# Kernel tuning notes

Hardware: AMD Instinct MI355X
Metric: run time of the kernel (lower is better)

The kernel has to match this reference:

```python
import jax, jax.numpy as jnp
import numpy as np

N_NODES = 100000
N_EDGES = 1600000
IN_FEATS, HIDDEN, N_CLASSES = 128, 64, 16


def gcn_layer(x, src, dst, W, b, n_nodes):
    # DGL GraphConv, norm='both': h = D_in^{-1/2} A (D_out^{-1/2} x) W + b
    # (W applied before aggregation since in_feats > out_feats, as DGL does)
    ones = jnp.ones((src.shape[0],), dtype=x.dtype)
    deg_out = jax.ops.segment_sum(ones, src, num_segments=n_nodes)
    deg_in = jax.ops.segment_sum(ones, dst, num_segments=n_nodes)
    norm_src = jax.lax.rsqrt(jnp.clip(deg_out, 1.0))  # [N]
    norm_dst = jax.lax.rsqrt(jnp.clip(deg_in, 1.0))   # [N]
    h = (x * norm_src[:, None]) @ W                    # [N, out]
    msgs = h[src]                                      # [E, out] gather
    agg = jax.ops.segment_sum(msgs, dst, num_segments=n_nodes)  # [N, out]
    return agg * norm_dst[:, None] + b


def setup_inputs() -> dict:
    key = jax.random.key(0)
    k1, k2, k3, k4, k5, k6, k7 = jax.random.split(key, 7)
    x = jax.random.normal(k1, (N_NODES, IN_FEATS), dtype=jnp.float32)
    src = jax.random.randint(k2, (N_EDGES,), 0, N_NODES, dtype=jnp.int32)
    dst = jax.random.randint(k3, (N_EDGES,), 0, N_NODES, dtype=jnp.int32)
    s1 = 1.0 / np.sqrt(IN_FEATS)
    s2 = 1.0 / np.sqrt(HIDDEN)
    W1 = jax.random.uniform(k4, (IN_FEATS, HIDDEN), jnp.float32, -s1, s1)
    b1 = jnp.zeros((HIDDEN,), dtype=jnp.float32)
    W2 = jax.random.uniform(k5, (HIDDEN, N_CLASSES), jnp.float32, -s2, s2)
    b2 = jnp.zeros((N_CLASSES,), dtype=jnp.float32)
    return {"x": x, "src": src, "dst": dst, "W1": W1, "b1": b1, "W2": W2, "b2": b2}


def reference(x, src, dst, W1, b1, W2, b2):
    h = gcn_layer(x, src, dst, W1, b1, N_NODES)
    h = jax.nn.relu(h)
    h = gcn_layer(h, src, dst, W2, b2, N_NODES)
    return jax.nn.softmax(h, axis=-1)  # [N, num_classes]
```

## Files before the change

kernel.cpp:

```cpp
#include <hip/hip_runtime.h>
#include <hip/hip_fp16.h>
#include <math.h>


constexpr int N_NODES = 100000;
constexpr int N_EDGES = 1600000;
constexpr int IN_F    = 128;
constexpr int HID     = 64;
constexpr int NC      = 16;

constexpr int NB_D   = 391;
constexpr int STR    = 4608;
constexpr int NBLK_P = 256;
constexpr int EPB    = N_EDGES / NBLK_P;
constexpr int CAPB   = 64;
constexpr int CSTR   = 16;

typedef _Float16 f16x8 __attribute__((ext_vector_type(8)));
typedef _Float16 f16x4 __attribute__((ext_vector_type(4)));
typedef float    f32x4 __attribute__((ext_vector_type(4)));

__global__ __launch_bounds__(512) void k_init(int* __restrict__ cursD,
                                              int* __restrict__ cursS) {
    int t = threadIdx.x;
    if (t < NB_D) {
        cursD[t * CSTR] = t * STR;
        cursS[t * CSTR] = t * STR;
    }
}

__global__ __launch_bounds__(1024) void k_part(const int* __restrict__ src,
                                               const int* __restrict__ dst,
                                               int* __restrict__ cursD,
                                               int* __restrict__ cursS,
                                               unsigned int* __restrict__ ebufD,
                                               unsigned char* __restrict__ ebufS) {
    __shared__ unsigned int  bufD[NB_D * CAPB];
    __shared__ unsigned char bufS[NB_D * CAPB];
    __shared__ int cD[NB_D], cS[NB_D], baseD[NB_D], baseS[NB_D];
    const int t = threadIdx.x, b = blockIdx.x;
    for (int i = t; i < NB_D; i += 1024) { cD[i] = 0; cS[i] = 0; }
    __syncthreads();
    const int beg = b * EPB, end = beg + EPB;
    for (int i = beg + t; i < end; i += 1024) {
        int d = dst[i], s = src[i];
        int bD = d >> 8;
        int c  = atomicAdd(&cD[bD], 1);
        if (c < CAPB) bufD[(bD << 6) + c] = ((unsigned)(d & 255) << 17) | (unsigned)s;
        int bS = s >> 8;
        int c2 = atomicAdd(&cS[bS], 1);
        if (c2 < CAPB) bufS[(bS << 6) + c2] = (unsigned char)(s & 255);
    }
    __syncthreads();
    for (int i = t; i < NB_D; i += 1024) {
        int c = min(cD[i], CAPB);
        cD[i] = c;
        baseD[i] = atomicAdd(&cursD[i * CSTR], c);
        int c2 = min(cS[i], CAPB);
        cS[i] = c2;
        baseS[i] = atomicAdd(&cursS[i * CSTR], c2);
    }
    __syncthreads();
    for (int slot = t; slot < NB_D * CAPB; slot += 1024) {
        int bk = slot >> 6, idx = slot & 63;
        if (idx < cD[bk]) ebufD[baseD[bk] + idx] = bufD[slot];
    }
    for (int slot = t; slot < NB_D * CAPB; slot += 1024) {
        int bk = slot >> 6, idx = slot & 63;
        if (idx < cS[bk]) ebufS[baseS[bk] + idx] = bufS[slot];
    }
}

__global__ __launch_bounds__(256) void k_bmerge(const int* __restrict__ cursD,
                                                const int* __restrict__ cursS,
                                                const unsigned int* __restrict__ ebufD,
                                                const unsigned char* __restrict__ ebufS,
                                                int* __restrict__ row_start,
                                                int* __restrict__ row_end,
                                                float* __restrict__ norm_dst,
                                                float* __restrict__ norm_src,
                                                int* __restrict__ csr_src) {
    __shared__ int cnt[256];
    __shared__ int curs[256];
    __shared__ int wsum[4];
    const int t = threadIdx.x;
    int b = blockIdx.x;
    if (b < NB_D) {
        const int beg = b * STR, end = cursD[b * CSTR];
        cnt[t] = 0;
        __syncthreads();
        for (int i = beg + t; i < end; i += 256)
            atomicAdd(&cnt[ebufD[i] >> 17], 1);
        __syncthreads();
        int x = cnt[t];
        int v = x;
        int lane = t & 63, wid = t >> 6;
        #pragma unroll
        for (int d = 1; d < 64; d <<= 1) { int u = __shfl_up(v, d, 64); if (lane >= d) v += u; }
        if (lane == 63) wsum[wid] = v;
        __syncthreads();
        int woff = 0;
        for (int w = 0; w < wid; ++w) woff += wsum[w];
        int rs = woff + v - x;
        int node = b * 256 + t;
        if (node < N_NODES) {
            row_start[node] = beg + rs;
            row_end[node]   = beg + rs + x;
            norm_dst[node]  = 1.0f / sqrtf(fmaxf((float)x, 1.0f));
        }
        curs[t] = beg + rs;
        __syncthreads();
        for (int i = beg + t; i < end; i += 256) {
            unsigned int e = ebufD[i];
            int pos = atomicAdd(&curs[e >> 17], 1);
            csr_src[pos] = (int)(e & 0x1FFFFu);
        }
    } else {
        b -= NB_D;
        const int beg = b * STR, end = cursS[b * CSTR];
        cnt[t] = 0;
        __syncthreads();
        for (int i = beg + t; i < end; i += 256)
            atomicAdd(&cnt[ebufS[i]], 1);
        __syncthreads();
        int node = b * 256 + t;
        if (node < N_NODES)
            norm_src[node] = 1.0f / sqrtf(fmaxf((float)cnt[t], 1.0f));
    }
}

constexpr int PADK = 136;
__global__ __launch_bounds__(256) void k_gemm1(
        const float* __restrict__ x, const float* __restrict__ W1,
        const float* __restrict__ norm_src, __half* __restrict__ h1h) {
    __shared__ _Float16 xh[64 * PADK];
    __shared__ _Float16 wt[64 * PADK];
    const int t = threadIdx.x;
    const int row0 = blockIdx.x * 64;
    for (int i = t; i < 64 * 32; i += 256) {
        int c4 = i & 31, rr = i >> 5;
        int gr = row0 + rr;
        float4 v = (gr < N_NODES) ? *(const float4*)&x[(size_t)gr * IN_F + c4 * 4]
                                  : float4{0.f, 0.f, 0.f, 0.f};
        f16x4 hv;
        hv[0] = (_Float16)v.x; hv[1] = (_Float16)v.y;
        hv[2] = (_Float16)v.z; hv[3] = (_Float16)v.w;
        *(f16x4*)&xh[rr * PADK + c4 * 4] = hv;
    }
    for (int i = t; i < 64 * 32; i += 256) {
        int n = i & 63, kq = i >> 6;
        int k0 = kq * 4;
        f16x4 hv;
        #pragma unroll
        for (int j = 0; j < 4; ++j)
            hv[j] = (_Float16)W1[(size_t)(k0 + j) * HID + n];
        *(f16x4*)&wt[n * PADK + k0] = hv;
    }
    __syncthreads();
    const int w = t >> 6;
    const int l = t & 63;
    const int m = l & 15, q = l >> 4;
    f32x4 acc0 = {0,0,0,0}, acc1 = {0,0,0,0}, acc2 = {0,0,0,0}, acc3 = {0,0,0,0};
    #pragma unroll
    for (int kc = 0; kc < 4; ++kc) {
        f16x8 af = *(const f16x8*)&xh[(16 * w + m) * PADK + kc * 32 + q * 8];
        f16x8 b0 = *(const f16x8*)&wt[( 0 + m) * PADK + kc * 32 + q * 8];
        f16x8 b1 = *(const f16x8*)&wt[(16 + m) * PADK + kc * 32 + q * 8];
        f16x8 b2 = *(const f16x8*)&wt[(32 + m) * PADK + kc * 32 + q * 8];
        f16x8 b3 = *(const f16x8*)&wt[(48 + m) * PADK + kc * 32 + q * 8];
        acc0 = __builtin_amdgcn_mfma_f32_16x16x32_f16(af, b0, acc0, 0, 0, 0);
        acc1 = __builtin_amdgcn_mfma_f32_16x16x32_f16(af, b1, acc1, 0, 0, 0);
        acc2 = __builtin_amdgcn_mfma_f32_16x16x32_f16(af, b2, acc2, 0, 0, 0);
        acc3 = __builtin_amdgcn_mfma_f32_16x16x32_f16(af, b3, acc3, 0, 0, 0);
    }
    _Float16* out = (_Float16*)h1h;
    #pragma unroll
    for (int r = 0; r < 4; ++r) {
        int row_g = row0 + 16 * w + q * 4 + r;
        if (row_g < N_NODES) {
            float ns = norm_src[row_g];
            size_t base = (size_t)row_g * HID + m;
            out[base +  0] = (_Float16)(acc0[r] * ns);
            out[base + 16] = (_Float16)(acc1[r] * ns);
            out[base + 32] = (_Float16)(acc2[r] * ns);
            out[base + 48] = (_Float16)(acc3[r] * ns);
        }
    }
}

__global__ __launch_bounds__(256) void k_agg1(
        const int* __restrict__ row_start, const int* __restrict__ row_end,
        const int* __restrict__ csr_src, const __half* __restrict__ h1h,
        const float* __restrict__ nd, const float* __restrict__ ns,
        const float* __restrict__ b1, const float* __restrict__ W2,
        __half* __restrict__ h2h) {
    __shared__ float W2s[64 * 17];
    const int t = threadIdx.x;
    for (int i = t; i < HID * NC; i += 256) {
        int k = i >> 4, j = i & 15;
        W2s[k * 17 + j] = W2[i];
    }
    __syncthreads();
    int node = blockIdx.x * 16 + (t >> 4);
    int q = t & 15;
    if (node >= N_NODES) return;
    int beg = row_start[node], end = row_end[node];
    float4 acc = {0.f, 0.f, 0.f, 0.f};
    int p = beg;
    for (; p + 8 <= end; p += 8) {
        float2 g[8];
        #pragma unroll
        for (int u = 0; u < 8; ++u) {
            int s = csr_src[p + u];
            g[u] = *(const float2*)&h1h[(size_t)s * HID + q * 4];
        }
        #pragma unroll
        for (int u = 0; u < 8; ++u) {
            float2 f0 = __half22float2(*(__half2*)&g[u].x);
            float2 f1 = __half22float2(*(__half2*)&g[u].y);
            acc.x += f0.x; acc.y += f0.y; acc.z += f1.x; acc.w += f1.y;
        }
    }
    for (; p < end; ++p) {
        int s = csr_src[p];
        float2 raw = *(const float2*)&h1h[(size_t)s * HID + q * 4];
        float2 f0 = __half22float2(*(__half2*)&raw.x);
        float2 f1 = __half22float2(*(__half2*)&raw.y);
        acc.x += f0.x; acc.y += f0.y; acc.z += f1.x; acc.w += f1.y;
    }
    float n = nd[node];
    float4 bb = *(const float4*)&b1[q * 4];
    float v0 = fmaxf(acc.x * n + bb.x, 0.f);
    float v1 = fmaxf(acc.y * n + bb.y, 0.f);
    float v2 = fmaxf(acc.z * n + bb.z, 0.f);
    float v3 = fmaxf(acc.w * n + bb.w, 0.f);
    float part[16];
    const float* w0 = &W2s[(4 * q + 0) * 17];
    const float* w1 = &W2s[(4 * q + 1) * 17];
    const float* w2 = &W2s[(4 * q + 2) * 17];
    const float* w3 = &W2s[(4 * q + 3) * 17];
    #pragma unroll
    for (int j = 0; j < 16; ++j)
        part[j] = v0 * w0[j] + v1 * w1[j] + v2 * w2[j] + v3 * w3[j];
    #pragma unroll
    for (int d = 1; d < 16; d <<= 1) {
        #pragma unroll
        for (int j = 0; j < 16; ++j)
            part[j] += __shfl_xor(part[j], d, 16);
    }
    float nsv = ns[node];
    ((_Float16*)h2h)[(size_t)node * NC + q] = (_Float16)(part[q] * nsv);
}

__global__ __launch_bounds__(256) void k_agg2(
        const int* __restrict__ row_start, const int* __restrict__ row_end,
        const int* __restrict__ csr_src, const __half* __restrict__ h2h,
        const float* __restrict__ nd, const float* __restrict__ b2,
        float* __restrict__ out) {
    int t = threadIdx.x;
    int node = blockIdx.x * 128 + (t >> 1);
    int sub = t & 1;
    if (node >= N_NODES) return;
    int beg = row_start[node], end = row_end[node];
    float acc[8] = {0,0,0,0,0,0,0,0};
    int p = beg;
    for (; p + 8 <= end; p += 8) {
        float4 g[8];
        #pragma unroll
        for (int u = 0; u < 8; ++u) {
            int s = csr_src[p + u];
            g[u] = *(const float4*)&h2h[(size_t)s * NC + sub * 8];
        }
        #pragma unroll
        for (int u = 0; u < 8; ++u) {
            const __half2* hh = (const __half2*)&g[u];
            #pragma unroll
            for (int j = 0; j < 4; ++j) {
                float2 f = __half22float2(hh[j]);
                acc[j * 2 + 0] += f.x; acc[j * 2 + 1] += f.y;
            }
        }
    }
    for (; p < end; ++p) {
        int s = csr_src[p];
        float4 g = *(const float4*)&h2h[(size_t)s * NC + sub * 8];
        const __half2* hh = (const __half2*)&g;
        #pragma unroll
        for (int j = 0; j < 4; ++j) {
            float2 f = __half22float2(hh[j]);
            acc[j * 2 + 0] += f.x; acc[j * 2 + 1] += f.y;
        }
    }
    float n = nd[node];
    float v[8];
    #pragma unroll
    for (int j = 0; j < 8; ++j) v[j] = acc[j] * n + b2[sub * 8 + j];
    float m = v[0];
    #pragma unroll
    for (int j = 1; j < 8; ++j) m = fmaxf(m, v[j]);
    m = fmaxf(m, __shfl_xor(m, 1, 2));
    float e[8]; float s = 0.f;
    #pragma unroll
    for (int j = 0; j < 8; ++j) { e[j] = __expf(v[j] - m); s += e[j]; }
    s += __shfl_xor(s, 1, 2);
    float inv = 1.0f / s;
    float4 o0 = { e[0]*inv, e[1]*inv, e[2]*inv, e[3]*inv };
    float4 o1 = { e[4]*inv, e[5]*inv, e[6]*inv, e[7]*inv };
    *(float4*)&out[(size_t)node * NC + sub * 8 + 0] = o0;
    *(float4*)&out[(size_t)node * NC + sub * 8 + 4] = o1;
}

extern "C" void kernel_launch(void* const* d_in, const int* in_sizes, int n_in,
                              void* d_out, int out_size, void* d_ws, size_t ws_size,
                              hipStream_t stream) {
    const float* x   = (const float*)d_in[0];
    const int*   src = (const int*)  d_in[1];
    const int*   dst = (const int*)  d_in[2];
    const float* W1  = (const float*)d_in[3];
    const float* b1  = (const float*)d_in[4];
    const float* W2  = (const float*)d_in[5];
    const float* b2  = (const float*)d_in[6];
    float* out = (float*)d_out;

    const size_t N = N_NODES;
    float* ws       = (float*)d_ws;
    int*   wsI      = (int*)d_ws;
    float* norm_src = ws;
    float* norm_dst = ws + N;
    __half* h1h     = (__half*)(ws + 2 * N);
    __half* h2h     = (__half*)(ws + 34 * N);
    unsigned int*  ebufD = (unsigned int*)(wsI + 66 * N);
    unsigned char* ebufS = (unsigned char*)(wsI + 66 * N + NB_D * STR);
    int*   row_st   = wsI + 130 * N;
    int*   row_en   = wsI + 131 * N;
    int*   cursD    = wsI + 132 * N;
    int*   cursS    = wsI + 132 * N + 8192;
    int*   csr_src  = wsI + 132 * N + 16384;

    k_init<<<1, 512, 0, stream>>>(cursD, cursS);
    k_part<<<NBLK_P, 1024, 0, stream>>>(src, dst, cursD, cursS, ebufD, ebufS);
    k_bmerge<<<2 * NB_D, 256, 0, stream>>>(cursD, cursS, ebufD, ebufS,
                                           row_st, row_en, norm_dst, norm_src,
                                           csr_src);
    k_gemm1<<<(N_NODES + 63) / 64, 256, 0, stream>>>(x, W1, norm_src, h1h);
    k_agg1<<<(N_NODES + 15) / 16, 256, 0, stream>>>(row_st, row_en, csr_src, h1h,
                                                    norm_dst, norm_src, b1, W2, h2h);
    k_agg2<<<(N_NODES + 127) / 128, 256, 0, stream>>>(row_st, row_en, csr_src, h2h,
                                                      norm_dst, b2, out);
}
```

Measured before the change: 221.3 us.

## Widen agg1 gathers to 16B per lane and replace shuffle reduction with LDS matvec

Layer-1 aggregation now uses 8 lanes per node, each gathering 8 halves (16 bytes) per neighbor instead of 16 lanes with 4 halves. This gives 32 nodes per block and fewer load instructions per edge. The post-aggregation ReLU result is staged in shared memory so each lane computes two output classes directly against a transposed W2. That removes the 64-step xor-shuffle butterfly reduction, at the cost of extra LDS traffic. The bounds check is dropped because N_NODES divides evenly by 32.

Result: faster. 205.5 us (-7.1%).

```diff
diff --git a/kernel.cpp b/kernel.cpp
--- a/kernel.cpp
+++ b/kernel.cpp
@@ -194,62 +194,77 @@
         const float* __restrict__ nd, const float* __restrict__ ns,
         const float* __restrict__ b1, const float* __restrict__ W2,
         __half* __restrict__ h2h) {
-    __shared__ float W2s[64 * 17];
+    __shared__ float W2t[16 * 68];
+    __shared__ float rb[32 * 68];
     const int t = threadIdx.x;
     for (int i = t; i < HID * NC; i += 256) {
-        int k = i >> 4, j = i & 15;
-        W2s[k * 17 + j] = W2[i];
-    }
-    __syncthreads();
-    int node = blockIdx.x * 16 + (t >> 4);
-    int q = t & 15;
-    if (node >= N_NODES) return;
-    int beg = row_start[node], end = row_end[node];
-    float4 acc = {0.f, 0.f, 0.f, 0.f};
+        int k = i >> 4, c = i & 15;
+        W2t[c * 68 + k] = W2[i];
+    }
+    __syncthreads();
+    const int w = t >> 6, l = t & 63;
+    const int g = l >> 3, j = l & 7;
+    const int nl = w * 8 + g;
+    const int node = blockIdx.x * 32 + nl;
+    const int beg = row_start[node], end = row_end[node];
+    float a0=0,a1=0,a2=0,a3=0,a4=0,a5=0,a6=0,a7=0;
     int p = beg;
     for (; p + 8 <= end; p += 8) {
-        float2 g[8];
+        float4 g4[8];
         #pragma unroll
         for (int u = 0; u < 8; ++u) {
             int s = csr_src[p + u];
-            g[u] = *(const float2*)&h1h[(size_t)s * HID + q * 4];
+            g4[u] = *(const float4*)&h1h[(size_t)s * HID + j * 8];
         }
         #pragma unroll
         for (int u = 0; u < 8; ++u) {
-            float2 f0 = __half22float2(*(__half2*)&g[u].x);
-            float2 f1 = __half22float2(*(__half2*)&g[u].y);
-            acc.x += f0.x; acc.y += f0.y; acc.z += f1.x; acc.w += f1.y;
+            const __half2* hh = (const __half2*)&g4[u];
+            float2 f0 = __half22float2(hh[0]);
+            float2 f1 = __half22float2(hh[1]);
+            float2 f2 = __half22float2(hh[2]);
+            float2 f3 = __half22float2(hh[3]);
+            a0 += f0.x; a1 += f0.y; a2 += f1.x; a3 += f1.y;
+            a4 += f2.x; a5 += f2.y; a6 += f3.x; a7 += f3.y;
         }
     }
     for (; p < end; ++p) {
         int s = csr_src[p];
-        float2 raw = *(const float2*)&h1h[(size_t)s * HID + q * 4];
-        float2 f0 = __half22float2(*(__half2*)&raw.x);
-        float2 f1 = __half22float2(*(__half2*)&raw.y);
-        acc.x += f0.x; acc.y += f0.y; acc.z += f1.x; acc.w += f1.y;
-    }
-    float n = nd[node];
-    float4 bb = *(const float4*)&b1[q * 4];
-    float v0 = fmaxf(acc.x * n + bb.x, 0.f);
-    float v1 = fmaxf(acc.y * n + bb.y, 0.f);
-    float v2 = fmaxf(acc.z * n + bb.z, 0.f);
-    float v3 = fmaxf(acc.w * n + bb.w, 0.f);
-    float part[16];
-    const float* w0 = &W2s[(4 * q + 0) * 17];
-    const float* w1 = &W2s[(4 * q + 1) * 17];
-    const float* w2 = &W2s[(4 * q + 2) * 17];
-    const float* w3 = &W2s[(4 * q + 3) * 17];
-    #pragma unroll
-    for (int j = 0; j < 16; ++j)
-        part[j] = v0 * w0[j] + v1 * w1[j] + v2 * w2[j] + v3 * w3[j];
-    #pragma unroll
-    for (int d = 1; d < 16; d <<= 1) {
-        #pragma unroll
-        for (int j = 0; j < 16; ++j)
-            part[j] += __shfl_xor(part[j], d, 16);
-    }
-    float nsv = ns[node];
-    ((_Float16*)h2h)[(size_t)node * NC + q] = (_Float16)(part[q] * nsv);
+        float4 g4 = *(const float4*)&h1h[(size_t)s * HID + j * 8];
+        const __half2* hh = (const __half2*)&g4;
+        float2 f0 = __half22float2(hh[0]);
+        float2 f1 = __half22float2(hh[1]);
+        float2 f2 = __half22float2(hh[2]);
+        float2 f3 = __half22float2(hh[3]);
+        a0 += f0.x; a1 += f0.y; a2 += f1.x; a3 += f1.y;
+        a4 += f2.x; a5 += f2.y; a6 += f3.x; a7 += f3.y;
+    }
+    const float n = nd[node];
+    const float4 bb0 = *(const float4*)&b1[j * 8 + 0];
+    const float4 bb1 = *(const float4*)&b1[j * 8 + 4];
+    float4 v0, v1;
+    v0.x = fmaxf(a0 * n + bb0.x, 0.f);
+    v0.y = fmaxf(a1 * n + bb0.y, 0.f);
+    v0.z = fmaxf(a2 * n + bb0.z, 0.f);
+    v0.w = fmaxf(a3 * n + bb0.w, 0.f);
+    v1.x = fmaxf(a4 * n + bb1.x, 0.f);
+    v1.y = fmaxf(a5 * n + bb1.y, 0.f);
+    v1.z = fmaxf(a6 * n + bb1.z, 0.f);
+    v1.w = fmaxf(a7 * n + bb1.w, 0.f);
+    *(float4*)&rb[nl * 68 + j * 8 + 0] = v0;
+    *(float4*)&rb[nl * 68 + j * 8 + 4] = v1;
+    float o0 = 0.f, o1 = 0.f;
+    #pragma unroll
+    for (int k4 = 0; k4 < 16; ++k4) {
+        float4 r  = *(float4*)&rb[nl * 68 + k4 * 4];
+        float4 wa = *(float4*)&W2t[j * 68 + k4 * 4];
+        float4 wb = *(float4*)&W2t[(j + 8) * 68 + k4 * 4];
+        o0 += r.x * wa.x + r.y * wa.y + r.z * wa.z + r.w * wa.w;
+        o1 += r.x * wb.x + r.y * wb.y + r.z * wb.z + r.w * wb.w;
+    }
+    const float nsv = ns[node];
+    _Float16* o = (_Float16*)h2h;
+    o[(size_t)node * NC + j]     = (_Float16)(o0 * nsv);
+    o[(size_t)node * NC + j + 8] = (_Float16)(o1 * nsv);
 }
 
 __global__ __launch_bounds__(256) void k_agg2(
@@ -343,8 +358,8 @@
                                            row_st, row_en, norm_dst, norm_src,
                                            csr_src);
     k_gemm1<<<(N_NODES + 63) / 64, 256, 0, stream>>>(x, W1, norm_src, h1h);
-    k_agg1<<<(N_NODES + 15) / 16, 256, 0, stream>>>(row_st, row_en, csr_src, h1h,
-                                                    norm_dst, norm_src, b1, W2, h2h);
+    k_agg1<<<N_NODES / 32, 256, 0, stream>>>(row_st, row_en, csr_src, h1h,
+                                             norm_dst, norm_src, b1, W2, h2h);
     k_agg2<<<(N_NODES + 127) / 128, 256, 0, stream>>>(row_st, row_en, csr_src, h2h,
                                                       norm_dst, b2, out);
 }
```
